# Performance work log

Measured on AMD Instinct MI355X. Metric: run time of the kernel, lower is better.

The kernel has to match this reference:

```python
import jax, jax.numpy as jnp
import numpy as np

D = 256      # d_v
FF = 512     # ff_dim = max(hidden, d_v)
H = 4        # num_heads
K = 8        # max_set_size
L = 64       # subset universe length
NC = 32768   # n_chains
NB = 4096    # n_batch
EPS = 1e-8   # module eps for masked-mean denom


def setup_inputs() -> dict:
    key = jax.random.key(0)
    ks = jax.random.split(key, 24)
    s = 0.02
    mask = jax.random.randint(ks[2], (NC, L), 0, 2).astype(bool)
    inp = {
        "v": jax.random.normal(ks[0], (NB, L, D), jnp.float32),
        "batch_idx": jax.random.randint(ks[1], (NC,), 0, NB),
        "mask": mask,
        "count": mask.sum(axis=1).astype(jnp.float32),
        "pos_embed": jnp.zeros((1, K, D), jnp.float32),
        "ln1_w": jnp.ones((D,), jnp.float32),
        "ln1_b": jnp.zeros((D,), jnp.float32),
        "in_proj_w": jax.random.normal(ks[3], (3 * D, D), jnp.float32) * s,
        "in_proj_b": jnp.zeros((3 * D,), jnp.float32),
        "out_proj_w": jax.random.normal(ks[4], (D, D), jnp.float32) * s,
        "out_proj_b": jnp.zeros((D,), jnp.float32),
        "ln2_w": jnp.ones((D,), jnp.float32),
        "ln2_b": jnp.zeros((D,), jnp.float32),
        "ff1_w": jax.random.normal(ks[5], (FF, D), jnp.float32) * s,
        "ff1_b": jnp.zeros((FF,), jnp.float32),
        "ff2_w": jax.random.normal(ks[6], (D, FF), jnp.float32) * s,
        "ff2_b": jnp.zeros((D,), jnp.float32),
        "o1_w": jax.random.normal(ks[7], (FF, D + 1), jnp.float32) * s,
        "o1_b": jnp.zeros((FF,), jnp.float32),
        "o2_w": jax.random.normal(ks[8], (D, FF), jnp.float32) * s,
        "o2_b": jnp.zeros((D,), jnp.float32),
    }
    return inp


def _layernorm(x, w, b, eps=1e-5):
    mu = x.mean(-1, keepdims=True)
    var = ((x - mu) ** 2).mean(-1, keepdims=True)
    return (x - mu) * jax.lax.rsqrt(var + eps) * w + b


def reference(v, batch_idx, mask, count, pos_embed, ln1_w, ln1_b, in_proj_w,
              in_proj_b, out_proj_w, out_proj_b, ln2_w, ln2_b, ff1_w, ff1_b,
              ff2_w, ff2_b, o1_w, o1_b, o2_w, o2_b):
    nc, Lm = mask.shape
    # --- topk subset select (index-order packing) ---
    pos = jnp.arange(Lm, dtype=jnp.float32)
    scores = mask.astype(jnp.float32) * (float(Lm) - pos)[None, :]
    top_scores, top_idx = jax.lax.top_k(scores, K)
    picked0 = top_scores > 0
    sortable = jnp.where(picked0, top_idx, Lm)
    sortable = jnp.sort(sortable, axis=1)
    picked = sortable < Lm                       # [NC,K]
    safe_idx = jnp.where(picked, sortable, 0)
    # fused gather: chain_v[c, i] = v[batch_idx[c], i]
    packed = v[batch_idx[:, None], safe_idx]     # [NC,K,D]
    packed = packed * picked[..., None].astype(packed.dtype)
    x = packed + pos_embed[:, :K, :]
    # key padding mask; un-mask position 0 for fully-empty sets
    kpm = ~picked
    empty = jnp.all(kpm, axis=1)
    kpm = kpm.at[:, 0].set(jnp.where(empty, False, kpm[:, 0]))
    # --- one pre-norm transformer encoder layer ---
    h = _layernorm(x, ln1_w, ln1_b)
    qkv = h @ in_proj_w.T + in_proj_b
    q, k_, vv = jnp.split(qkv, 3, axis=-1)
    hd = D // H
    def heads(t):
        return t.reshape(nc, K, H, hd).transpose(0, 2, 1, 3)
    q, k_, vv = heads(q), heads(k_), heads(vv)
    att = jnp.einsum('bhqd,bhkd->bhqk', q, k_) / jnp.sqrt(jnp.float32(hd))
    att = jnp.where(kpm[:, None, None, :], -jnp.inf, att)
    att = jax.nn.softmax(att, axis=-1)
    ao = jnp.einsum('bhqk,bhkd->bhqd', att, vv).transpose(0, 2, 1, 3).reshape(nc, K, D)
    x = x + ao @ out_proj_w.T + out_proj_b
    h2 = _layernorm(x, ln2_w, ln2_b)
    x = x + jax.nn.gelu(h2 @ ff1_w.T + ff1_b, approximate=False) @ ff2_w.T + ff2_b
    # --- masked mean pool ---
    pf = picked.astype(x.dtype)
    denom = jnp.maximum(pf.sum(axis=1, keepdims=True), EPS)
    pooled = (x * pf[..., None]).sum(axis=1) / denom
    pooled = jnp.where(picked.any(axis=1, keepdims=True), pooled, jnp.zeros_like(pooled))
    # --- concat log(1+|S|) and project ---
    feat = jnp.concatenate([pooled, jnp.log1p(count)[:, None]], axis=-1)
    return jax.nn.gelu(feat @ o1_w.T + o1_b, approximate=False) @ o2_w.T + o2_b
```

## Files before the change

### kernel.cpp

```cpp
#include <hip/hip_runtime.h>
#include <hip/hip_bf16.h>
#include <math.h>

typedef short short8 __attribute__((ext_vector_type(8)));
typedef short short4v __attribute__((ext_vector_type(4)));
typedef float f32x4 __attribute__((ext_vector_type(4)));

#define NCC  32768
#define G    4

#define G1_OFF 0
#define G2_OFF 196608
#define G3_OFF 262144
#define G4_OFF 393216
#define O1_OFF 524288
#define O2_OFF 655360
#define SWZ_SHORTS 786432
#define W256_BYTE_OFF (SWZ_SHORTS * 2)
#define FLAG_BYTE_OFF (W256_BYTE_OFF + 2048)

__device__ __forceinline__ float gelu_f(float x) {
    return x * 0.5f * (1.0f + erff(x * 0.70710678118654752f));
}
__device__ __forceinline__ unsigned short f2bf(float f) {
    __hip_bfloat16 h = __float2bfloat16(f);
    return *reinterpret_cast<unsigned short*>(&h);
}
__device__ __forceinline__ int aswz(int row, int scol) {
    return row * 256 + (scol ^ ((row & 7) << 3));
}
__device__ __forceinline__ int qswz(int row, int scol) {
    return row * 512 + (scol ^ ((row & 7) << 3));
}
__device__ __forceinline__ int vtswz(int d, int j) {
    return d * 32 + (j ^ ((d & 7) << 2));
}

template<int KTS>
__device__ __forceinline__ void load_bgrp(short8 (&b)[KTS], const unsigned short* __restrict__ base) {
    #pragma unroll
    for (int kt = 0; kt < KTS; kt++)
        b[kt] = *reinterpret_cast<const short8*>(base + (size_t)kt * 512);
}

__global__ void conv_weights(const float* __restrict__ w1, const float* __restrict__ w2,
                             const float* __restrict__ w3, const float* __restrict__ w4,
                             const float* __restrict__ o1, const float* __restrict__ o2,
                             unsigned short* __restrict__ dst, float* __restrict__ w256) {
    int i = blockIdx.x * 256 + threadIdx.x;
    if (i < 98304) {
        const float* src; int kts, sk, base;
        if (i < 24576)      { src = w1; kts = 8;  sk = 256; base = 0; }
        else if (i < 32768) { src = w2; kts = 8;  sk = 256; base = 24576; }
        else if (i < 49152) { src = w3; kts = 8;  sk = 256; base = 32768; }
        else if (i < 65536) { src = w4; kts = 16; sk = 512; base = 49152; }
        else if (i < 81920) { src = o1; kts = 8;  sk = 257; base = 65536; }
        else                { src = o2; kts = 16; sk = 512; base = 81920; }
        int li   = i - base;
        int lane = li & 63;
        int fi   = li >> 6;
        int kt   = fi % kts;
        int nt   = fi / kts;
        int col  = nt * 16 + (lane & 15);
        int k    = kt * 32 + (lane >> 4) * 8;
        const float* s = src + (size_t)col * sk + k;
        unsigned short* d = dst + (size_t)i * 8;
        #pragma unroll
        for (int e = 0; e < 8; e++) d[e] = f2bf(s[e]);
    } else if (i < 98816) {
        int c = i - 98304;
        w256[c] = o1[(size_t)c * 257 + 256];
    }
}

__global__ void detect_mask_fmt(const unsigned int* __restrict__ mw, int nwords, int* __restrict__ flag) {
    __shared__ int s_bad_int, s_bad_float;
    if (threadIdx.x == 0) { s_bad_int = 0; s_bad_float = 0; }
    __syncthreads();
    int bad_int = 0, bad_float = 0;
    for (int i = threadIdx.x; i < nwords; i += blockDim.x) {
        unsigned int w = mw[i];
        if (w > 1u) bad_int = 1;
        if (w != 0u && w != 0x3F800000u) bad_float = 1;
    }
    if (bad_int)   atomicOr(&s_bad_int, 1);
    if (bad_float) atomicOr(&s_bad_float, 1);
    __syncthreads();
    if (threadIdx.x == 0)
        *flag = (!s_bad_int) ? 0 : ((!s_bad_float) ? 2 : 1);
}

__global__ __launch_bounds__(256, 2)
void tsa_main(const float* __restrict__ v,
              const int* __restrict__ batch_idx,
              const void* __restrict__ mask,
              const float* __restrict__ pos_embed,
              const float* __restrict__ ln1_w, const float* __restrict__ ln1_b,
              const float* __restrict__ in_proj_b,
              const float* __restrict__ out_proj_b,
              const float* __restrict__ ln2_w, const float* __restrict__ ln2_b,
              const float* __restrict__ ff1_b, const float* __restrict__ ff2_b,
              const unsigned short* __restrict__ wb,
              const int* __restrict__ mask_flag,
              float* __restrict__ out)
{
    __shared__ unsigned short qkbuf[32 * 512];
    __shared__ unsigned short abuf[32 * 256];
    __shared__ unsigned short attw_s[2][4][16][16];
    __shared__ int s_idx[G][8];
    __shared__ int s_m[G];
    __shared__ int s_bi[G];

    float* lnred = reinterpret_cast<float*>(qkbuf);
    float* px2   = reinterpret_cast<float*>(qkbuf + 2048);
    float* pgff  = reinterpret_cast<float*>(qkbuf + 8192);

    const int tid  = threadIdx.x;
    const int lane = tid & 63;
    const int wid  = tid >> 6;
    const int cq   = lane >> 4;
    const int cc   = lane & 15;
    const int cg0  = blockIdx.x * G;
    const int pair = wid >> 1;

    f32x4 xr[2][4];

    {
        int mf = *mask_flag;
        size_t base = (size_t)(cg0 + wid) * 64 + lane;
        int bit;
        if (mf == 0)      bit = ((const int*)mask)[base] != 0;
        else if (mf == 2) bit = ((const float*)mask)[base] != 0.0f;
        else              bit = ((const unsigned char*)mask)[base] != 0;
        unsigned long long bal = __ballot(bit);
        if (lane == 0) {
            int mm = 0; unsigned long long b = bal;
            while (b && mm < 8) { s_idx[wid][mm++] = __ffsll(b) - 1; b &= (b - 1); }
            for (int t = mm; t < 8; t++) s_idx[wid][t] = 0;
            s_m[wid]  = mm;
            s_bi[wid] = batch_idx[cg0 + wid];
        }
    }
    __syncthreads();

    auto do_gather = [&]() {
        #pragma unroll
        for (int mt = 0; mt < 2; mt++) {
            int c  = 2 * mt + (cq >> 1);
            int m  = s_m[c];
            int bi = s_bi[c];
            #pragma unroll
            for (int rr = 0; rr < 4; rr++) {
                int rowin = (cq & 1) * 4 + rr;
                int vidx  = s_idx[c][rowin];
                #pragma unroll
                for (int nt = 0; nt < 4; nt++) {
                    int col  = wid * 64 + nt * 16 + cc;
                    float pe = pos_embed[rowin * 256 + col];
                    float val = (rowin < m) ? v[((size_t)bi * 64 + vidx) * 256 + col] : 0.0f;
                    xr[mt][nt][rr] = val + pe;
                }
            }
        }
    };

    auto do_ln = [&](const float* __restrict__ lw, const float* __restrict__ lb) {
        float sm[2][4], sq[2][4];
        #pragma unroll
        for (int mt = 0; mt < 2; mt++)
            #pragma unroll
            for (int rr = 0; rr < 4; rr++) {
                float s = 0.f, q = 0.f;
                #pragma unroll
                for (int nt = 0; nt < 4; nt++) {
                    float x = xr[mt][nt][rr];
                    s += x; q += x * x;
                }
                sm[mt][rr] = s; sq[mt][rr] = q;
            }
        #pragma unroll
        for (int off = 1; off < 16; off <<= 1) {
            #pragma unroll
            for (int mt = 0; mt < 2; mt++)
                #pragma unroll
                for (int rr = 0; rr < 4; rr++) {
                    sm[mt][rr] += __shfl_xor(sm[mt][rr], off);
                    sq[mt][rr] += __shfl_xor(sq[mt][rr], off);
                }
        }
        if (cc == 0) {
            #pragma unroll
            for (int mt = 0; mt < 2; mt++)
                #pragma unroll
                for (int rr = 0; rr < 4; rr++) {
                    int row = mt * 16 + cq * 4 + rr;
                    lnred[(wid * 32 + row) * 2 + 0] = sm[mt][rr];
                    lnred[(wid * 32 + row) * 2 + 1] = sq[mt][rr];
                }
        }
        __syncthreads();
        float mu[2][4], rs[2][4];
        #pragma unroll
        for (int mt = 0; mt < 2; mt++)
            #pragma unroll
            for (int rr = 0; rr < 4; rr++) {
                int row = mt * 16 + cq * 4 + rr;
                float S = 0.f, Q = 0.f;
                #pragma unroll
                for (int w = 0; w < 4; w++) {
                    S += lnred[(w * 32 + row) * 2 + 0];
                    Q += lnred[(w * 32 + row) * 2 + 1];
                }
                float m_ = S * (1.0f / 256.0f);
                mu[mt][rr] = m_;
                rs[mt][rr] = rsqrtf(Q * (1.0f / 256.0f) - m_ * m_ + 1e-5f);
            }
        #pragma unroll
        for (int nt = 0; nt < 4; nt++) {
            int col = wid * 64 + nt * 16 + cc;
            float w_ = lw[col], b_ = lb[col];
            #pragma unroll
            for (int mt = 0; mt < 2; mt++)
                #pragma unroll
                for (int rr = 0; rr < 4; rr++) {
                    int row = mt * 16 + cq * 4 + rr;
                    abuf[aswz(row, col)] = f2bf((xr[mt][nt][rr] - mu[mt][rr]) * rs[mt][rr] * w_ + b_);
                }
        }
        __syncthreads();
    };

    auto load_a_abuf = [&](short8 (&a0)[8], short8 (&a1)[8]) {
        #pragma unroll
        for (int kt = 0; kt < 8; kt++) {
            a0[kt] = *reinterpret_cast<const short8*>(&abuf[aswz(cc,      kt * 32 + cq * 8)]);
            a1[kt] = *reinterpret_cast<const short8*>(&abuf[aswz(16 + cc, kt * 32 + cq * 8)]);
        }
    };

    do_gather();
    do_ln(ln1_w, ln1_b);

    {
        short8 a0[8], a1[8];
        load_a_abuf(a0, a1);
        __syncthreads();

        auto gbase = [&](int g) {
            int nt = g >> 1, kh = g & 1;
            int gnt = (nt < 8) ? (wid * 8 + nt) : (32 + wid * 4 + (nt - 8));
            return wb + G1_OFF + ((size_t)gnt * 8 + kh * 4) * 512 + lane * 8;
        };
        short8 bb[2][4];
        load_bgrp<4>(bb[0], gbase(0));
        f32x4 c0, c1;
        #pragma unroll
        for (int nt = 0; nt < 12; nt++) {
            #pragma unroll
            for (int kh = 0; kh < 2; kh++) {
                int g = nt * 2 + kh;
                if (g + 1 < 24) load_bgrp<4>(bb[(g + 1) & 1], gbase(g + 1));
                if (kh == 0) {
                    float b = (nt < 8) ? in_proj_b[wid * 128 + nt * 16 + cc]
                                       : in_proj_b[512 + wid * 64 + (nt - 8) * 16 + cc];
                    c0 = (f32x4){b, b, b, b};
                    c1 = (f32x4){b, b, b, b};
                }
                __builtin_amdgcn_s_setprio(1);
                #pragma unroll
                for (int kt = 0; kt < 4; kt++) {
                    c0 = __builtin_amdgcn_mfma_f32_16x16x32_bf16(a0[kh * 4 + kt], bb[g & 1][kt], c0, 0, 0, 0);
                    c1 = __builtin_amdgcn_mfma_f32_16x16x32_bf16(a1[kh * 4 + kt], bb[g & 1][kt], c1, 0, 0, 0);
                }
                __builtin_amdgcn_s_setprio(0);
            }
            if (nt < 8) {
                int col = wid * 128 + nt * 16 + cc;
                #pragma unroll
                for (int r = 0; r < 4; r++) {
                    qkbuf[qswz(cq * 4 + r, col)]      = f2bf(c0[r]);
                    qkbuf[qswz(16 + cq * 4 + r, col)] = f2bf(c1[r]);
                }
            } else {
                int d = wid * 64 + (nt - 8) * 16 + cc;
                short4v p0, p1;
                #pragma unroll
                for (int r = 0; r < 4; r++) { p0[r] = (short)f2bf(c0[r]); p1[r] = (short)f2bf(c1[r]); }
                *reinterpret_cast<short4v*>(&abuf[vtswz(d, cq * 4)])      = p0;
                *reinterpret_cast<short4v*>(&abuf[vtswz(d, 16 + cq * 4)]) = p1;
            }
        }
    }
    __syncthreads();

    do_gather();

    {
        #pragma unroll
        for (int hj = 0; hj < 2; hj++) {
            int h = (wid & 1) * 2 + hj;
            f32x4 c = {0.f, 0.f, 0.f, 0.f};
            #pragma unroll
            for (int kt = 0; kt < 2; kt++) {
                short8 qa = *reinterpret_cast<const short8*>(&qkbuf[qswz(pair * 16 + cc, h * 64 + cq * 8 + kt * 32)]);
                short8 kb = *reinterpret_cast<const short8*>(&qkbuf[qswz(pair * 16 + cc, 256 + h * 64 + cq * 8 + kt * 32)]);
                c = __builtin_amdgcn_mfma_f32_16x16x32_bf16(qa, kb, c, 0, 0, 0);
            }
            int jhalf = cc >> 3, jloc = cc & 7;
            #pragma unroll
            for (int r = 0; r < 4; r++) {
                int q = cq * 4 + r;
                int qhalf = q >> 3;
                int m = s_m[pair * 2 + qhalf];
                bool valid = (jhalf == qhalf) && (jloc < m);
                float s = valid ? c[r] * 0.125f : -1e30f;
                float mx = s;
                mx = fmaxf(mx, __shfl_xor(mx, 1));
                mx = fmaxf(mx, __shfl_xor(mx, 2));
                mx = fmaxf(mx, __shfl_xor(mx, 4));
                float e = valid ? __expf(s - mx) : 0.f;
                float se = e;
                se += __shfl_xor(se, 1);
                se += __shfl_xor(se, 2);
                se += __shfl_xor(se, 4);
                attw_s[pair][h][q][cc] = f2bf((se > 0.f) ? e / se : 0.f);
            }
        }
    }
    __syncthreads();

    {
        int jbg = pair * 16 + (cq & 1) * 8;
        #pragma unroll
        for (int hj = 0; hj < 2; hj++) {
            int h = (wid & 1) * 2 + hj;
            short8 pa;
            if (cq < 2) pa = *reinterpret_cast<const short8*>(&attw_s[pair][h][cc][cq * 8]);
            else        pa = (short8)((short)0);
            #pragma unroll
            for (int t = 0; t < 4; t++) {
                int d = h * 64 + t * 16 + cc;
                short4v lo = *reinterpret_cast<const short4v*>(&abuf[vtswz(d, jbg)]);
                short4v hi = *reinterpret_cast<const short4v*>(&abuf[vtswz(d, jbg + 4)]);
                union { short8 vv; short4v half2[2]; } u;
                u.half2[0] = lo; u.half2[1] = hi;
                f32x4 c = {0.f, 0.f, 0.f, 0.f};
                c = __builtin_amdgcn_mfma_f32_16x16x32_bf16(pa, u.vv, c, 0, 0, 0);
                #pragma unroll
                for (int r = 0; r < 4; r++)
                    qkbuf[qswz(pair * 16 + cq * 4 + r, d)] = f2bf(c[r]);
            }
        }
    }
    __syncthreads();

    {
        #pragma unroll
        for (int nt = 0; nt < 4; nt++) {
            float b = out_proj_b[wid * 64 + nt * 16 + cc];
            #pragma unroll
            for (int r = 0; r < 4; r++) { xr[0][nt][r] += b; xr[1][nt][r] += b; }
        }
        auto gbase = [&](int g) {
            int kh = g >> 2, nt = g & 3;
            return wb + G2_OFF + ((size_t)(wid * 4 + nt) * 8 + kh * 4) * 512 + lane * 8;
        };
        short8 bb[2][4];
        load_bgrp<4>(bb[0], gbase(0));
        #pragma unroll
        for (int kh = 0; kh < 2; kh++) {
            short8 a0h[4], a1h[4];
            #pragma unroll
            for (int kt = 0; kt < 4; kt++) {
                a0h[kt] = *reinterpret_cast<const short8*>(&qkbuf[qswz(cc,      kh * 128 + kt * 32 + cq * 8)]);
                a1h[kt] = *reinterpret_cast<const short8*>(&qkbuf[qswz(16 + cc, kh * 128 + kt * 32 + cq * 8)]);
            }
            #pragma unroll
            for (int nt = 0; nt < 4; nt++) {
                int g = kh * 4 + nt;
                if (g + 1 < 8) load_bgrp<4>(bb[(g + 1) & 1], gbase(g + 1));
                __builtin_amdgcn_s_setprio(1);
                #pragma unroll
                for (int kt = 0; kt < 4; kt++) {
                    xr[0][nt] = __builtin_amdgcn_mfma_f32_16x16x32_bf16(a0h[kt], bb[g & 1][kt], xr[0][nt], 0, 0, 0);
                    xr[1][nt] = __builtin_amdgcn_mfma_f32_16x16x32_bf16(a1h[kt], bb[g & 1][kt], xr[1][nt], 0, 0, 0);
                }
                __builtin_amdgcn_s_setprio(0);
            }
        }
    }
    __syncthreads();

    #pragma unroll
    for (int mt = 0; mt < 2; mt++) {
        int c = 2 * mt + (cq >> 1);
        int m = s_m[c];
        #pragma unroll
        for (int nt = 0; nt < 4; nt++) {
            float p = 0.f;
            #pragma unroll
            for (int rr = 0; rr < 4; rr++)
                if ((cq & 1) * 4 + rr < m) p += xr[mt][nt][rr];
            p += __shfl_xor(p, 16);
            if ((cq & 1) == 0) {
                int col = wid * 64 + nt * 16 + cc;
                px2[c * 256 + col] = p;
            }
        }
    }

    do_ln(ln2_w, ln2_b);

    {
        short8 a0[8], a1[8];
        load_a_abuf(a0, a1);
        auto gbase = [&](int g) {
            int nt = g >> 1, kh = g & 1;
            return wb + G3_OFF + ((size_t)(wid * 8 + nt) * 8 + kh * 4) * 512 + lane * 8;
        };
        short8 bb[2][4];
        load_bgrp<4>(bb[0], gbase(0));
        f32x4 c0, c1;
        #pragma unroll
        for (int nt = 0; nt < 8; nt++) {
            #pragma unroll
            for (int kh = 0; kh < 2; kh++) {
                int g = nt * 2 + kh;
                if (g + 1 < 16) load_bgrp<4>(bb[(g + 1) & 1], gbase(g + 1));
                if (kh == 0) {
                    float b = ff1_b[wid * 128 + nt * 16 + cc];
                    c0 = (f32x4){b, b, b, b};
                    c1 = (f32x4){b, b, b, b};
                }
                __builtin_amdgcn_s_setprio(1);
                #pragma unroll
                for (int kt = 0; kt < 4; kt++) {
                    c0 = __builtin_amdgcn_mfma_f32_16x16x32_bf16(a0[kh * 4 + kt], bb[g & 1][kt], c0, 0, 0, 0);
                    c1 = __builtin_amdgcn_mfma_f32_16x16x32_bf16(a1[kh * 4 + kt], bb[g & 1][kt], c1, 0, 0, 0);
                }
                __builtin_amdgcn_s_setprio(0);
            }
            int col = wid * 128 + nt * 16 + cc;
            float s0 = 0.f, s1 = 0.f;
            int m0 = s_m[cq >> 1];
            int m1 = s_m[2 + (cq >> 1)];
            #pragma unroll
            for (int r = 0; r < 4; r++) {
                float g0 = gelu_f(c0[r]);
                float g1 = gelu_f(c1[r]);
                if ((cq & 1) * 4 + r < m0) s0 += g0;
                if ((cq & 1) * 4 + r < m1) s1 += g1;
            }
            s0 += __shfl_xor(s0, 16);
            s1 += __shfl_xor(s1, 16);
            if ((cq & 1) == 0) {
                pgff[(cq >> 1) * 512 + col]       = s0;
                pgff[(2 + (cq >> 1)) * 512 + col] = s1;
            }
        }
    }
    __syncthreads();

    {
        auto gbase = [&](int g) {
            int kh = g >> 2, nt = g & 3;
            return wb + G4_OFF + ((size_t)(wid * 4 + nt) * 16 + kh * 4) * 512 + lane * 8;
        };
        short8 bb[2][4];
        load_bgrp<4>(bb[0], gbase(0));
        f32x4 acc[4];
        #pragma unroll
        for (int nt = 0; nt < 4; nt++) acc[nt] = (f32x4){0.f, 0.f, 0.f, 0.f};
        #pragma unroll
        for (int kh = 0; kh < 4; kh++) {
            short8 af[4];
            #pragma unroll
            for (int kt = 0; kt < 4; kt++) {
                short8 t = (short8)((short)0);
                if (cc < 4) {
                    const float* src = &pgff[cc * 512 + (kh * 4 + kt) * 32 + cq * 8];
                    #pragma unroll
                    for (int e = 0; e < 8; e++) t[e] = (short)f2bf(src[e]);
                }
                af[kt] = t;
            }
            #pragma unroll
            for (int nt = 0; nt < 4; nt++) {
                int g = kh * 4 + nt;
                if (g + 1 < 16) load_bgrp<4>(bb[(g + 1) & 1], gbase(g + 1));
                __builtin_amdgcn_s_setprio(1);
                #pragma unroll
                for (int kt = 0; kt < 4; kt++)
                    acc[nt] = __builtin_amdgcn_mfma_f32_16x16x32_bf16(af[kt], bb[g & 1][kt], acc[nt], 0, 0, 0);
                __builtin_amdgcn_s_setprio(0);
            }
        }
        if (cq == 0) {
            #pragma unroll
            for (int nt = 0; nt < 4; nt++) {
                int col = wid * 64 + nt * 16 + cc;
                float b4 = ff2_b[col];
                #pragma unroll
                for (int r = 0; r < 4; r++) {
                    int m = s_m[r];
                    float val = 0.f;
                    if (m > 0) val = (px2[r * 256 + col] + acc[nt][r]) / (float)m + b4;
                    out[(size_t)(cg0 + r) * 256 + col] = val;
                }
            }
        }
    }
}

__global__ __launch_bounds__(256, 2)
void tsa_head(const float* __restrict__ count,
              const float* __restrict__ o1_b, const float* __restrict__ o2_b,
              const unsigned short* __restrict__ wb, const float* __restrict__ w256,
              float* __restrict__ out)
{
    __shared__ unsigned short fbuf[32 * 256];
    __shared__ unsigned short gbuf[32 * 512];
    __shared__ float cbuf[32];

    const int tid  = threadIdx.x;
    const int lane = tid & 63;
    const int wid  = tid >> 6;
    const int cq   = lane >> 4;
    const int cc   = lane & 15;
    const int c0b  = blockIdx.x * 32;

    for (int i = tid; i < 32 * 256; i += 256) {
        int row = i >> 8, col = i & 255;
        fbuf[aswz(row, col)] = f2bf(out[(size_t)(c0b + row) * 256 + col]);
    }
    if (tid < 32) cbuf[tid] = log1pf(count[c0b + tid]);
    __syncthreads();

    short8 a0[8], a1[8];
    #pragma unroll
    for (int kt = 0; kt < 8; kt++) {
        a0[kt] = *reinterpret_cast<const short8*>(&fbuf[aswz(cc,      kt * 32 + cq * 8)]);
        a1[kt] = *reinterpret_cast<const short8*>(&fbuf[aswz(16 + cc, kt * 32 + cq * 8)]);
    }

    {
        auto gbase = [&](int g) {
            int nt = g >> 1, kh = g & 1;
            return wb + O1_OFF + ((size_t)(wid * 8 + nt) * 8 + kh * 4) * 512 + lane * 8;
        };
        short8 bb[2][4];
        load_bgrp<4>(bb[0], gbase(0));
        f32x4 c0, c1;
        #pragma unroll
        for (int nt = 0; nt < 8; nt++) {
            #pragma unroll
            for (int kh = 0; kh < 2; kh++) {
                int g = nt * 2 + kh;
                if (g + 1 < 16) load_bgrp<4>(bb[(g + 1) & 1], gbase(g + 1));
                if (kh == 0) {
                    float b = o1_b[wid * 128 + nt * 16 + cc];
                    c0 = (f32x4){b, b, b, b};
                    c1 = (f32x4){b, b, b, b};
                }
                __builtin_amdgcn_s_setprio(1);
                #pragma unroll
                for (int kt = 0; kt < 4; kt++) {
                    c0 = __builtin_amdgcn_mfma_f32_16x16x32_bf16(a0[kh * 4 + kt], bb[g & 1][kt], c0, 0, 0, 0);
                    c1 = __builtin_amdgcn_mfma_f32_16x16x32_bf16(a1[kh * 4 + kt], bb[g & 1][kt], c1, 0, 0, 0);
                }
                __builtin_amdgcn_s_setprio(0);
            }
            int col  = wid * 128 + nt * 16 + cc;
            float wc = w256[col];
            #pragma unroll
            for (int r = 0; r < 4; r++) {
                int r0 = cq * 4 + r, r1 = 16 + cq * 4 + r;
                gbuf[qswz(r0, col)] = f2bf(gelu_f(c0[r] + cbuf[r0] * wc));
                gbuf[qswz(r1, col)] = f2bf(gelu_f(c1[r] + cbuf[r1] * wc));
            }
        }
    }
    __syncthreads();

    {
        f32x4 c[4][2];
        #pragma unroll
        for (int nt = 0; nt < 4; nt++) {
            float b = o2_b[wid * 64 + nt * 16 + cc];
            c[nt][0] = (f32x4){b, b, b, b};
            c[nt][1] = (f32x4){b, b, b, b};
        }
        auto gbase = [&](int g) {
            int half = g >> 3, kh = (g >> 2) & 1, nt = g & 3;
            return wb + O2_OFF + ((size_t)(wid * 4 + nt) * 16 + half * 8 + kh * 4) * 512 + lane * 8;
        };
        short8 bb[2][4];
        load_bgrp<4>(bb[0], gbase(0));
        #pragma unroll
        for (int half = 0; half < 2; half++) {
            #pragma unroll
            for (int kh = 0; kh < 2; kh++) {
                short8 a0q[4], a1q[4];
                #pragma unroll
                for (int kt = 0; kt < 4; kt++) {
                    int scol = half * 256 + kh * 128 + kt * 32 + cq * 8;
                    a0q[kt] = *reinterpret_cast<const short8*>(&gbuf[qswz(cc,      scol)]);
                    a1q[kt] = *reinterpret_cast<const short8*>(&gbuf[qswz(16 + cc, scol)]);
                }
                #pragma unroll
                for (int nt = 0; nt < 4; nt++) {
                    int g = half * 8 + kh * 4 + nt;
                    if (g + 1 < 16) load_bgrp<4>(bb[(g + 1) & 1], gbase(g + 1));
                    __builtin_amdgcn_s_setprio(1);
                    #pragma unroll
                    for (int kt = 0; kt < 4; kt++) {
                        c[nt][0] = __builtin_amdgcn_mfma_f32_16x16x32_bf16(a0q[kt], bb[g & 1][kt], c[nt][0], 0, 0, 0);
                        c[nt][1] = __builtin_amdgcn_mfma_f32_16x16x32_bf16(a1q[kt], bb[g & 1][kt], c[nt][1], 0, 0, 0);
                    }
                    __builtin_amdgcn_s_setprio(0);
                }
            }
        }
        #pragma unroll
        for (int nt = 0; nt < 4; nt++) {
            int col = wid * 64 + nt * 16 + cc;
            #pragma unroll
            for (int r = 0; r < 4; r++) {
                out[(size_t)(c0b + cq * 4 + r) * 256 + col]      = c[nt][0][r];
                out[(size_t)(c0b + 16 + cq * 4 + r) * 256 + col] = c[nt][1][r];
            }
        }
    }
}

extern "C" void kernel_launch(void* const* d_in, const int* in_sizes, int n_in,
                              void* d_out, int out_size, void* d_ws, size_t ws_size,
                              hipStream_t stream) {
    const float* v          = (const float*)d_in[0];
    const int*   batch_idx  = (const int*)d_in[1];
    const void*  mask       = d_in[2];
    const float* count      = (const float*)d_in[3];
    const float* pos_embed  = (const float*)d_in[4];
    const float* ln1_w      = (const float*)d_in[5];
    const float* ln1_b      = (const float*)d_in[6];
    const float* in_proj_w  = (const float*)d_in[7];
    const float* in_proj_b  = (const float*)d_in[8];
    const float* out_proj_w = (const float*)d_in[9];
    const float* out_proj_b = (const float*)d_in[10];
    const float* ln2_w      = (const float*)d_in[11];
    const float* ln2_b      = (const float*)d_in[12];
    const float* ff1_w      = (const float*)d_in[13];
    const float* ff1_b      = (const float*)d_in[14];
    const float* ff2_w      = (const float*)d_in[15];
    const float* ff2_b      = (const float*)d_in[16];
    const float* o1_w       = (const float*)d_in[17];
    const float* o1_b       = (const float*)d_in[18];
    const float* o2_w       = (const float*)d_in[19];
    const float* o2_b       = (const float*)d_in[20];
    float* out = (float*)d_out;

    unsigned short* wb = (unsigned short*)d_ws;
    float* w256 = (float*)((char*)d_ws + W256_BYTE_OFF);
    int* flag   = (int*)((char*)d_ws + FLAG_BYTE_OFF);

    conv_weights<<<387, 256, 0, stream>>>(in_proj_w, out_proj_w, ff1_w, ff2_w, o1_w, o2_w, wb, w256);
    detect_mask_fmt<<<1, 256, 0, stream>>>((const unsigned int*)mask, 16384, flag);
    tsa_main<<<NCC / G, 256, 0, stream>>>(v, batch_idx, mask, pos_embed,
                                          ln1_w, ln1_b, in_proj_b, out_proj_b,
                                          ln2_w, ln2_b, ff1_b, ff2_b,
                                          wb, flag, out);
    tsa_head<<<NCC / 32, 256, 0, stream>>>(count, o1_b, o2_b, wb, w256, out);
}
```

Baseline: 570.0 us.

## Triple-buffer weight prefetch and restructure GEMM loops into K-half A-fragment chunks

Every weight-streaming GEMM stage now uses a three-deep register ring for B fragments, so prefetches run two groups ahead instead of one, giving global loads more time to land. The QK projection, FF1 and O1 GEMMs are reordered into two chunks of four N-tiles. Each chunk loads only half of the K-dimension A fragments at a time and accumulates eight tiles, which cuts live A registers. The V projection is split into its own loop. The cost is more accumulator and B-buffer registers, which may affect occupancy, and A fragments are re-read from LDS once per chunk.

Result: slower. 613.6 us (+7.6%).

```diff
diff --git a/kernel.cpp b/kernel.cpp
--- a/kernel.cpp
+++ b/kernel.cpp
@@ -237,58 +237,110 @@
             a1[kt] = *reinterpret_cast<const short8*>(&abuf[aswz(16 + cc, kt * 32 + cq * 8)]);
         }
     };
+    auto load_ah_abuf = [&](short8 (&a0h)[4], short8 (&a1h)[4], int kh) {
+        #pragma unroll
+        for (int kt = 0; kt < 4; kt++) {
+            a0h[kt] = *reinterpret_cast<const short8*>(&abuf[aswz(cc,      kh * 128 + kt * 32 + cq * 8)]);
+            a1h[kt] = *reinterpret_cast<const short8*>(&abuf[aswz(16 + cc, kh * 128 + kt * 32 + cq * 8)]);
+        }
+    };
+    auto load_ah_qk = [&](short8 (&a0h)[4], short8 (&a1h)[4], int so) {
+        #pragma unroll
+        for (int kt = 0; kt < 4; kt++) {
+            a0h[kt] = *reinterpret_cast<const short8*>(&qkbuf[qswz(cc,      so + kt * 32 + cq * 8)]);
+            a1h[kt] = *reinterpret_cast<const short8*>(&qkbuf[qswz(16 + cc, so + kt * 32 + cq * 8)]);
+        }
+    };
 
     do_gather();
     do_ln(ln1_w, ln1_b);
+
+    {
+        auto gbase = [&](int g) {
+            int chunk = g >> 3, kh = (g >> 2) & 1, nt4 = g & 3;
+            int gnt = wid * 8 + chunk * 4 + nt4;
+            return wb + G1_OFF + ((size_t)gnt * 8 + kh * 4) * 512 + lane * 8;
+        };
+        short8 bb[3][4];
+        load_bgrp<4>(bb[0], gbase(0));
+        load_bgrp<4>(bb[1], gbase(1));
+        #pragma unroll
+        for (int chunk = 0; chunk < 2; chunk++) {
+            f32x4 c[4][2];
+            #pragma unroll
+            for (int nt4 = 0; nt4 < 4; nt4++) {
+                float b = in_proj_b[wid * 128 + (chunk * 4 + nt4) * 16 + cc];
+                c[nt4][0] = (f32x4){b, b, b, b};
+                c[nt4][1] = (f32x4){b, b, b, b};
+            }
+            #pragma unroll
+            for (int kh = 0; kh < 2; kh++) {
+                short8 a0h[4], a1h[4];
+                load_ah_abuf(a0h, a1h, kh);
+                #pragma unroll
+                for (int nt4 = 0; nt4 < 4; nt4++) {
+                    int g = chunk * 8 + kh * 4 + nt4;
+                    if (g + 2 < 16) load_bgrp<4>(bb[(g + 2) % 3], gbase(g + 2));
+                    __builtin_amdgcn_s_setprio(1);
+                    #pragma unroll
+                    for (int kt = 0; kt < 4; kt++) {
+                        c[nt4][0] = __builtin_amdgcn_mfma_f32_16x16x32_bf16(a0h[kt], bb[g % 3][kt], c[nt4][0], 0, 0, 0);
+                        c[nt4][1] = __builtin_amdgcn_mfma_f32_16x16x32_bf16(a1h[kt], bb[g % 3][kt], c[nt4][1], 0, 0, 0);
+                    }
+                    __builtin_amdgcn_s_setprio(0);
+                }
+            }
+            #pragma unroll
+            for (int nt4 = 0; nt4 < 4; nt4++) {
+                int col = wid * 128 + (chunk * 4 + nt4) * 16 + cc;
+                #pragma unroll
+                for (int r = 0; r < 4; r++) {
+                    qkbuf[qswz(cq * 4 + r, col)]      = f2bf(c[nt4][0][r]);
+                    qkbuf[qswz(16 + cq * 4 + r, col)] = f2bf(c[nt4][1][r]);
+                }
+            }
+        }
+    }
 
     {
         short8 a0[8], a1[8];
         load_a_abuf(a0, a1);
         __syncthreads();
 
-        auto gbase = [&](int g) {
+        auto vbase = [&](int g) {
             int nt = g >> 1, kh = g & 1;
-            int gnt = (nt < 8) ? (wid * 8 + nt) : (32 + wid * 4 + (nt - 8));
+            int gnt = 32 + wid * 4 + nt;
             return wb + G1_OFF + ((size_t)gnt * 8 + kh * 4) * 512 + lane * 8;
         };
-        short8 bb[2][4];
-        load_bgrp<4>(bb[0], gbase(0));
+        short8 bb[3][4];
+        load_bgrp<4>(bb[0], vbase(0));
+        load_bgrp<4>(bb[1], vbase(1));
         f32x4 c0, c1;
         #pragma unroll
-        for (int nt = 0; nt < 12; nt++) {
+        for (int nt = 0; nt < 4; nt++) {
             #pragma unroll
             for (int kh = 0; kh < 2; kh++) {
                 int g = nt * 2 + kh;
-                if (g + 1 < 24) load_bgrp<4>(bb[(g + 1) & 1], gbase(g + 1));
+                if (g + 2 < 8) load_bgrp<4>(bb[(g + 2) % 3], vbase(g + 2));
                 if (kh == 0) {
-                    float b = (nt < 8) ? in_proj_b[wid * 128 + nt * 16 + cc]
-                                       : in_proj_b[512 + wid * 64 + (nt - 8) * 16 + cc];
+                    float b = in_proj_b[512 + wid * 64 + nt * 16 + cc];
                     c0 = (f32x4){b, b, b, b};
                     c1 = (f32x4){b, b, b, b};
                 }
                 __builtin_amdgcn_s_setprio(1);
                 #pragma unroll
                 for (int kt = 0; kt < 4; kt++) {
-                    c0 = __builtin_amdgcn_mfma_f32_16x16x32_bf16(a0[kh * 4 + kt], bb[g & 1][kt], c0, 0, 0, 0);
-                    c1 = __builtin_amdgcn_mfma_f32_16x16x32_bf16(a1[kh * 4 + kt], bb[g & 1][kt], c1, 0, 0, 0);
+                    c0 = __builtin_amdgcn_mfma_f32_16x16x32_bf16(a0[kh * 4 + kt], bb[g % 3][kt], c0, 0, 0, 0);
+                    c1 = __builtin_amdgcn_mfma_f32_16x16x32_bf16(a1[kh * 4 + kt], bb[g % 3][kt], c1, 0, 0, 0);
                 }
                 __builtin_amdgcn_s_setprio(0);
             }
-            if (nt < 8) {
-                int col = wid * 128 + nt * 16 + cc;
-                #pragma unroll
-                for (int r = 0; r < 4; r++) {
-                    qkbuf[qswz(cq * 4 + r, col)]      = f2bf(c0[r]);
-                    qkbuf[qswz(16 + cq * 4 + r, col)] = f2bf(c1[r]);
-                }
-            } else {
-                int d = wid * 64 + (nt - 8) * 16 + cc;
-                short4v p0, p1;
-                #pragma unroll
-                for (int r = 0; r < 4; r++) { p0[r] = (short)f2bf(c0[r]); p1[r] = (short)f2bf(c1[r]); }
-                *reinterpret_cast<short4v*>(&abuf[vtswz(d, cq * 4)])      = p0;
-                *reinterpret_cast<short4v*>(&abuf[vtswz(d, 16 + cq * 4)]) = p1;
-            }
+            int d = wid * 64 + nt * 16 + cc;
+            short4v p0, p1;
+            #pragma unroll
+            for (int r = 0; r < 4; r++) { p0[r] = (short)f2bf(c0[r]); p1[r] = (short)f2bf(c1[r]); }
+            *reinterpret_cast<short4v*>(&abuf[vtswz(d, cq * 4)])      = p0;
+            *reinterpret_cast<short4v*>(&abuf[vtswz(d, 16 + cq * 4)]) = p1;
         }
     }
     __syncthreads();
@@ -365,25 +417,22 @@
             int kh = g >> 2, nt = g & 3;
             return wb + G2_OFF + ((size_t)(wid * 4 + nt) * 8 + kh * 4) * 512 + lane * 8;
         };
-        short8 bb[2][4];
+        short8 bb[3][4];
         load_bgrp<4>(bb[0], gbase(0));
+        load_bgrp<4>(bb[1], gbase(1));
         #pragma unroll
         for (int kh = 0; kh < 2; kh++) {
             short8 a0h[4], a1h[4];
-            #pragma unroll
-            for (int kt = 0; kt < 4; kt++) {
-                a0h[kt] = *reinterpret_cast<const short8*>(&qkbuf[qswz(cc,      kh * 128 + kt * 32 + cq * 8)]);
-                a1h[kt] = *reinterpret_cast<const short8*>(&qkbuf[qswz(16 + cc, kh * 128 + kt * 32 + cq * 8)]);
-            }
+            load_ah_qk(a0h, a1h, kh * 128);
             #pragma unroll
             for (int nt = 0; nt < 4; nt++) {
                 int g = kh * 4 + nt;
-                if (g + 1 < 8) load_bgrp<4>(bb[(g + 1) & 1], gbase(g + 1));
+                if (g + 2 < 8) load_bgrp<4>(bb[(g + 2) % 3], gbase(g + 2));
                 __builtin_amdgcn_s_setprio(1);
                 #pragma unroll
                 for (int kt = 0; kt < 4; kt++) {
-                    xr[0][nt] = __builtin_amdgcn_mfma_f32_16x16x32_bf16(a0h[kt], bb[g & 1][kt], xr[0][nt], 0, 0, 0);
-                    xr[1][nt] = __builtin_amdgcn_mfma_f32_16x16x32_bf16(a1h[kt], bb[g & 1][kt], xr[1][nt], 0, 0, 0);
+                    xr[0][nt] = __builtin_amdgcn_mfma_f32_16x16x32_bf16(a0h[kt], bb[g % 3][kt], xr[0][nt], 0, 0, 0);
+                    xr[1][nt] = __builtin_amdgcn_mfma_f32_16x16x32_bf16(a1h[kt], bb[g % 3][kt], xr[1][nt], 0, 0, 0);
                 }
                 __builtin_amdgcn_s_setprio(0);
             }
@@ -412,50 +461,59 @@
     do_ln(ln2_w, ln2_b);
 
     {
-        short8 a0[8], a1[8];
-        load_a_abuf(a0, a1);
         auto gbase = [&](int g) {
-            int nt = g >> 1, kh = g & 1;
-            return wb + G3_OFF + ((size_t)(wid * 8 + nt) * 8 + kh * 4) * 512 + lane * 8;
+            int chunk = g >> 3, kh = (g >> 2) & 1, nt4 = g & 3;
+            int gnt = wid * 8 + chunk * 4 + nt4;
+            return wb + G3_OFF + ((size_t)gnt * 8 + kh * 4) * 512 + lane * 8;
         };
-        short8 bb[2][4];
+        short8 bb[3][4];
         load_bgrp<4>(bb[0], gbase(0));
-        f32x4 c0, c1;
-        #pragma unroll
-        for (int nt = 0; nt < 8; nt++) {
+        load_bgrp<4>(bb[1], gbase(1));
+        #pragma unroll
+        for (int chunk = 0; chunk < 2; chunk++) {
+            f32x4 c[4][2];
+            #pragma unroll
+            for (int nt4 = 0; nt4 < 4; nt4++) {
+                float b = ff1_b[wid * 128 + (chunk * 4 + nt4) * 16 + cc];
+                c[nt4][0] = (f32x4){b, b, b, b};
+                c[nt4][1] = (f32x4){b, b, b, b};
+            }
             #pragma unroll
             for (int kh = 0; kh < 2; kh++) {
-                int g = nt * 2 + kh;
-                if (g + 1 < 16) load_bgrp<4>(bb[(g + 1) & 1], gbase(g + 1));
-                if (kh == 0) {
-                    float b = ff1_b[wid * 128 + nt * 16 + cc];
-                    c0 = (f32x4){b, b, b, b};
-                    c1 = (f32x4){b, b, b, b};
-                }
-                __builtin_amdgcn_s_setprio(1);
-                #pragma unroll
-                for (int kt = 0; kt < 4; kt++) {
-                    c0 = __builtin_amdgcn_mfma_f32_16x16x32_bf16(a0[kh * 4 + kt], bb[g & 1][kt], c0, 0, 0, 0);
-                    c1 = __builtin_amdgcn_mfma_f32_16x16x32_bf16(a1[kh * 4 + kt], bb[g & 1][kt], c1, 0, 0, 0);
-                }
-                __builtin_amdgcn_s_setprio(0);
-            }
-            int col = wid * 128 + nt * 16 + cc;
-            float s0 = 0.f, s1 = 0.f;
+                short8 a0h[4], a1h[4];
+                load_ah_abuf(a0h, a1h, kh);
+                #pragma unroll
+                for (int nt4 = 0; nt4 < 4; nt4++) {
+                    int g = chunk * 8 + kh * 4 + nt4;
+                    if (g + 2 < 16) load_bgrp<4>(bb[(g + 2) % 3], gbase(g + 2));
+                    __builtin_amdgcn_s_setprio(1);
+                    #pragma unroll
+                    for (int kt = 0; kt < 4; kt++) {
+                        c[nt4][0] = __builtin_amdgcn_mfma_f32_16x16x32_bf16(a0h[kt], bb[g % 3][kt], c[nt4][0], 0, 0, 0);
+                        c[nt4][1] = __builtin_amdgcn_mfma_f32_16x16x32_bf16(a1h[kt], bb[g % 3][kt], c[nt4][1], 0, 0, 0);
+                    }
+                    __builtin_amdgcn_s_setprio(0);
+                }
+            }
             int m0 = s_m[cq >> 1];
             int m1 = s_m[2 + (cq >> 1)];
             #pragma unroll
-            for (int r = 0; r < 4; r++) {
-                float g0 = gelu_f(c0[r]);
-                float g1 = gelu_f(c1[r]);
-                if ((cq & 1) * 4 + r < m0) s0 += g0;
-                if ((cq & 1) * 4 + r < m1) s1 += g1;
-            }
-            s0 += __shfl_xor(s0, 16);
-            s1 += __shfl_xor(s1, 16);
-            if ((cq & 1) == 0) {
-                pgff[(cq >> 1) * 512 + col]       = s0;
-                pgff[(2 + (cq >> 1)) * 512 + col] = s1;
+            for (int nt4 = 0; nt4 < 4; nt4++) {
+                int col = wid * 128 + (chunk * 4 + nt4) * 16 + cc;
+                float s0 = 0.f, s1 = 0.f;
+                #pragma unroll
+                for (int r = 0; r < 4; r++) {
+                    float g0 = gelu_f(c[nt4][0][r]);
+                    float g1 = gelu_f(c[nt4][1][r]);
+                    if ((cq & 1) * 4 + r < m0) s0 += g0;
+                    if ((cq & 1) * 4 + r < m1) s1 += g1;
+                }
+                s0 += __shfl_xor(s0, 16);
+                s1 += __shfl_xor(s1, 16);
+                if ((cq & 1) == 0) {
+                    pgff[(cq >> 1) * 512 + col]       = s0;
+                    pgff[(2 + (cq >> 1)) * 512 + col] = s1;
+                }
             }
         }
     }
@@ -536,47 +594,55 @@
     if (tid < 32) cbuf[tid] = log1pf(count[c0b + tid]);
     __syncthreads();
 
-    short8 a0[8], a1[8];
-    #pragma unroll
-    for (int kt = 0; kt < 8; kt++) {
-        a0[kt] = *reinterpret_cast<const short8*>(&fbuf[aswz(cc,      kt * 32 + cq * 8)]);
-        a1[kt] = *reinterpret_cast<const short8*>(&fbuf[aswz(16 + cc, kt * 32 + cq * 8)]);
-    }
-
     {
         auto gbase = [&](int g) {
-            int nt = g >> 1, kh = g & 1;
-            return wb + O1_OFF + ((size_t)(wid * 8 + nt) * 8 + kh * 4) * 512 + lane * 8;
+            int chunk = g >> 3, kh = (g >> 2) & 1, nt4 = g & 3;
+            int gnt = wid * 8 + chunk * 4 + nt4;
+            return wb + O1_OFF + ((size_t)gnt * 8 + kh * 4) * 512 + lane * 8;
         };
-        short8 bb[2][4];
+        short8 bb[3][4];
         load_bgrp<4>(bb[0], gbase(0));
-        f32x4 c0, c1;
-        #pragma unroll
-        for (int nt = 0; nt < 8; nt++) {
+        load_bgrp<4>(bb[1], gbase(1));
+        #pragma unroll
+        for (int chunk = 0; chunk < 2; chunk++) {
+            f32x4 c[4][2];
+            #pragma unroll
+            for (int nt4 = 0; nt4 < 4; nt4++) {
+                float b = o1_b[wid * 128 + (chunk * 4 + nt4) * 16 + cc];
+                c[nt4][0] = (f32x4){b, b, b, b};
+                c[nt4][1] = (f32x4){b, b, b, b};
+            }
             #pragma unroll
             for (int kh = 0; kh < 2; kh++) {
-                int g = nt * 2 + kh;
-                if (g + 1 < 16) load_bgrp<4>(bb[(g + 1) & 1], gbase(g + 1));
-                if (kh == 0) {
-                    float b = o1_b[wid * 128 + nt * 16 + cc];
-                    c0 = (f32x4){b, b, b, b};
-                    c1 = (f32x4){b, b, b, b};
-                }
-                __builtin_amdgcn_s_setprio(1);
+                short8 a0h[4], a1h[4];
                 #pragma unroll
                 for (int kt = 0; kt < 4; kt++) {
-                    c0 = __builtin_amdgcn_mfma_f32_16x16x32_bf16(a0[kh * 4 + kt], bb[g & 1][kt], c0, 0, 0, 0);
-                    c1 = __builtin_amdgcn_mfma_f32_16x16x32_bf16(a1[kh * 4 + kt], bb[g & 1][kt], c1, 0, 0, 0);
-                }
-                __builtin_amdgcn_s_setprio(0);
-            }
-            int col  = wid * 128 + nt * 16 + cc;
-            float wc = w256[col];
-            #pragma unroll
-            for (int r = 0; r < 4; r++) {
-                int r0 = cq * 4 + r, r1 = 16 + cq * 4 + r;
-                gbuf[qswz(r0, col)] = f2bf(gelu_f(c0[r] + cbuf[r0] * wc));
-                gbuf[qswz(r1, col)] = f2bf(gelu_f(c1[r] + cbuf[r1] * wc));
+                    a0h[kt] = *reinterpret_cast<const short8*>(&fbuf[aswz(cc,      kh * 128 + kt * 32 + cq * 8)]);
+                    a1h[kt] = *reinterpret_cast<const short8*>(&fbuf[aswz(16 + cc, kh * 128 + kt * 32 + cq * 8)]);
+                }
+                #pragma unroll
+                for (int nt4 = 0; nt4 < 4; nt4++) {
+                    int g = chunk * 8 + kh * 4 + nt4;
+                    if (g + 2 < 16) load_bgrp<4>(bb[(g + 2) % 3], gbase(g + 2));
+                    __builtin_amdgcn_s_setprio(1);
+                    #pragma unroll
+                    for (int kt = 0; kt < 4; kt++) {
+                        c[nt4][0] = __builtin_amdgcn_mfma_f32_16x16x32_bf16(a0h[kt], bb[g % 3][kt], c[nt4][0], 0, 0, 0);
+                        c[nt4][1] = __builtin_amdgcn_mfma_f32_16x16x32_bf16(a1h[kt], bb[g % 3][kt], c[nt4][1], 0, 0, 0);
+                    }
+                    __builtin_amdgcn_s_setprio(0);
+                }
+            }
+            #pragma unroll
+            for (int nt4 = 0; nt4 < 4; nt4++) {
+                int col  = wid * 128 + (chunk * 4 + nt4) * 16 + cc;
+                float wc = w256[col];
+                #pragma unroll
+                for (int r = 0; r < 4; r++) {
+                    int r0 = cq * 4 + r, r1 = 16 + cq * 4 + r;
+                    gbuf[qswz(r0, col)] = f2bf(gelu_f(c[nt4][0][r] + cbuf[r0] * wc));
+                    gbuf[qswz(r1, col)] = f2bf(gelu_f(c[nt4][1][r] + cbuf[r1] * wc));
+                }
             }
         }
     }
@@ -594,8 +660,9 @@
             int half = g >> 3, kh = (g >> 2) & 1, nt = g & 3;
             return wb + O2_OFF + ((size_t)(wid * 4 + nt) * 16 + half * 8 + kh * 4) * 512 + lane * 8;
         };
-        short8 bb[2][4];
+        short8 bb[3][4];
         load_bgrp<4>(bb[0], gbase(0));
+        load_bgrp<4>(bb[1], gbase(1));
         #pragma unroll
         for (int half = 0; half < 2; half++) {
             #pragma unroll
@@ -610,12 +677,12 @@
                 #pragma unroll
                 for (int nt = 0; nt < 4; nt++) {
                     int g = half * 8 + kh * 4 + nt;
-                    if (g + 1 < 16) load_bgrp<4>(bb[(g + 1) & 1], gbase(g + 1));
+                    if (g + 2 < 16) load_bgrp<4>(bb[(g + 2) % 3], gbase(g + 2));
                     __builtin_amdgcn_s_setprio(1);
                     #pragma unroll
                     for (int kt = 0; kt < 4; kt++) {
-                        c[nt][0] = __builtin_amdgcn_mfma_f32_16x16x32_bf16(a0q[kt], bb[g & 1][kt], c[nt][0], 0, 0, 0);
-                        c[nt][1] = __builtin_amdgcn_mfma_f32_16x16x32_bf16(a1q[kt], bb[g & 1][kt], c[nt][1], 0, 0, 0);
+                        c[nt][0] = __builtin_amdgcn_mfma_f32_16x16x32_bf16(a0q[kt], bb[g % 3][kt], c[nt][0], 0, 0, 0);
+                        c[nt][1] = __builtin_amdgcn_mfma_f32_16x16x32_bf16(a1q[kt], bb[g % 3][kt], c[nt][1], 0, 0, 0);
                     }
                     __builtin_amdgcn_s_setprio(0);
                 }
```
